# Kernel tuning notes

Hardware: AMD Instinct MI355X
Metric: run time of the kernel (lower is better)

The kernel has to match this reference:

```python
import jax, jax.numpy as jnp
import numpy as np

D_MODEL = 1024
N_STATE = 64
BASEWIDTH = 3
BC_SCALE = (D_MODEL / BASEWIDTH) ** -0.5  # 'mup' mode width_mult**-0.5
RMS_EPS = 1.1920928955078125e-07  # torch.finfo(float32).eps (RMSNorm eps=None default)


def setup_inputs() -> dict:
    key = jax.random.key(0)
    k1, k2, k3, k4 = jax.random.split(key, 4)
    Bsz, L = 4, 2048
    u = jax.random.normal(k1, (Bsz, D_MODEL, L), dtype=jnp.float32)
    A = jax.random.uniform(k2, (N_STATE,), dtype=jnp.float32) * 0.1  # buffer: rand(N)*A_scale
    B = (jax.random.normal(k3, (N_STATE, D_MODEL), dtype=jnp.float32) + 0.1) * BC_SCALE
    C = (jax.random.normal(k4, (N_STATE, D_MODEL), dtype=jnp.float32) + 0.1) * BC_SCALE
    D = jnp.ones((D_MODEL,), dtype=jnp.float32)
    norm_w = jnp.ones((D_MODEL,), dtype=jnp.float32)
    return {"L": L, "u": u, "A": A, "B": B, "C": C, "D": D, "norm_w": norm_w}


def _ssm(u, A, B, C, D, norm_w):
    # u: [b, d, l]
    scale = BC_SCALE  # applied to Bu, Cu in 'mup' hyperparam mode
    Bu = jnp.einsum('nd,bdl->bnl', B, u) * scale  # [b, n, l]
    Cu = jnp.einsum('nd,bdl->bnl', C, u) * scale  # [b, n, l]
    b, d, l = u.shape
    # shifted_delta == 1 (delta path commented out in source), so
    # h_{t} = A * h_{t-1} + Bu[:, :, t] (outer) u[:, :, t]
    h0 = jnp.zeros((b, d, A.shape[0]), dtype=u.dtype)

    def step(h, xs):
        bu_t, cu_t, u_t = xs  # [b,n], [b,n], [b,d]
        h = h * A + u_t[:, :, None] * bu_t[:, None, :]  # [b, d, n]
        y_t = jnp.einsum('bn,bdn->bd', cu_t, h)
        return h, y_t

    xs = (jnp.moveaxis(Bu, 2, 0), jnp.moveaxis(Cu, 2, 0), jnp.moveaxis(u, 2, 0))
    _, y = jax.lax.scan(step, h0, xs)  # y: [l, b, d]
    y = jnp.moveaxis(y, 0, 2).transpose(1, 0, 2) if False else jnp.transpose(y, (1, 2, 0))  # [b, d, l]
    out = y + u * D[None, :, None]
    # RMSNorm over d_model (apply in [b, l, d] layout)
    x = jnp.transpose(out, (0, 2, 1))  # [b, l, d]
    ms = jnp.mean(x * x, axis=-1, keepdims=True)
    x = x * jax.lax.rsqrt(ms + RMS_EPS) * norm_w
    return jnp.transpose(x, (0, 2, 1))  # [b, d, l]


def reference(L, u, A, B, C, D, norm_w):
    del L  # sequence length == u.shape[-1]
    return _ssm(u, A, B, C, D, norm_w)
```

## Files before the change

### kernel.cpp

```cpp
#include <hip/hip_runtime.h>
#include <stdint.h>

#define DM 1024
#define LS 2048
#define RMS_EPS 1.1920928955078125e-07f
#define S2 0.0029296875f

typedef __attribute__((ext_vector_type(8))) short bf16x8;
typedef __attribute__((ext_vector_type(4))) float f32x4;

__device__ __forceinline__ unsigned short f2bf(float f) {
  uint32_t u = __builtin_bit_cast(uint32_t, f);
  u += 0x7FFFu + ((u >> 16) & 1u);
  return (unsigned short)(u >> 16);
}

__global__ __launch_bounds__(256) void k0_prep(const float* __restrict__ B,
                                               const float* __restrict__ C,
                                               unsigned short* __restrict__ Bbf) {
  int i4 = blockIdx.x * 256 + threadIdx.x;
  const float4* src = (i4 < 16384) ? (const float4*)B : (const float4*)C;
  float4 v = src[i4 & 16383];
  ushort4 o;
  o.x = f2bf(v.x); o.y = f2bf(v.y); o.z = f2bf(v.z); o.w = f2bf(v.w);
  ((ushort4*)Bbf)[i4] = o;
}

__global__ __launch_bounds__(1024) void kf(const float* __restrict__ u,
                                           const unsigned short* __restrict__ Bbf,
                                           const float* __restrict__ A,
                                           const float* __restrict__ Dv,
                                           const float* __restrict__ nw,
                                           float* __restrict__ out) {
  const int wg  = blockIdx.x;
  const int nbx = (wg & 7) * 64 + (wg >> 3);
  const int b   = nbx >> 7;
  const int t0  = (nbx & 127) << 4;
  const int tid = threadIdx.x;
  const int lane = tid & 63;
  const int w    = tid >> 6;
  const float* ub = u + (size_t)b * DM * LS;
  float* ob = out + (size_t)b * DM * LS;

  __shared__ __align__(16) char SMEM[65536];
  __shared__ __align__(16) float Bu[32][68];
  __shared__ __align__(16) float Cu[16][68];
  __shared__ __align__(16) float KwS[16][20];
  bf16x8 (*tile)[32]  = (bf16x8 (*)[32])SMEM;
  float (*y_lds)[1024] = (float (*)[1024])SMEM;
  float (*SS2)[20] = (float (*)[20])Cu;
  float *rsq       = (float*)((char*)Cu + 1280);

  {
    const int h16 = w >> 3;
    const int ks  = w & 7;
    const int tb  = lane >> 5;
    const int kg  = (lane >> 2) & 7;
    const int lq  = lane & 3;
    const int kbase = 128*ks + 64*tb + 8*kg;
    const int gcol  = t0 - 16 + 16*h16 + 4*lq;
    float4 vv[8];
    if (gcol >= 0) {
      #pragma unroll
      for (int r = 0; r < 8; ++r)
        vv[r] = *(const float4*)(ub + (size_t)(kbase + r) * LS + gcol);
    } else {
      #pragma unroll
      for (int r = 0; r < 8; ++r) vv[r] = make_float4(0.f, 0.f, 0.f, 0.f);
    }
    const int k8 = 16*ks + 8*tb + kg;
    #pragma unroll
    for (int c = 0; c < 4; ++c) {
      union { bf16x8 v; unsigned short s[8]; } t8;
      #pragma unroll
      for (int r = 0; r < 8; ++r) t8.s[r] = f2bf(((const float*)&vv[r])[c]);
      tile[k8][16*h16 + ((4*lq + c) ^ (k8 & 3))] = t8.v;
    }
  }
  __syncthreads();

  {
    const int nn = lane & 15, q = lane >> 4;
    const int wm = w & 7, wn = w >> 3;
    const unsigned short* arow = Bbf + (size_t)(16*wm + nn) * DM;
    f32x4 acc = {};
    #pragma unroll 4
    for (int it = 0; it < 32; ++it) {
      bf16x8 bfrag = tile[4*it + q][16*wn + (nn ^ q)];
      bf16x8 afrag = *(const bf16x8*)(arow + 32*it + 8*q);
      acc = __builtin_amdgcn_mfma_f32_16x16x32_bf16(afrag, bfrag, acc, 0, 0, 0);
    }
    const int ucol = 16*wn + nn;
    const int bcr  = 16*wm + 4*q;
    if (wm < 4)       *(f32x4*)&Bu[ucol][bcr]            = acc;
    else if (wn == 1) *(f32x4*)&Cu[ucol - 16][bcr - 64]  = acc;
  }
  __syncthreads();

  {
    const int p  = lane & 15;
    const int tl = lane >> 4;
    const int jq = w & 3;
    const int t  = 4*(w >> 2) + tl;
    const float4 cu = *(const float4*)&Cu[t][4*p];
    const float4 aa = *(const float4*)(A + 4*p);
    float a2x = aa.x*aa.x, a2y = aa.y*aa.y, a2z = aa.z*aa.z, a2w = aa.w*aa.w;
    float a4x = a2x*a2x,  a4y = a2y*a2y,  a4z = a2z*a2z,  a4w = a2w*a2w;
    float a8x = a4x*a4x,  a8y = a4y*a4y,  a8z = a4z*a4z,  a8w = a4w*a4w;
    float acx = a8x*a4x,  acy = a8y*a4y,  acz = a8z*a4z,  acw = a8w*a4w;
    float apx = (jq==0)?1.f:(jq==1)?a4x:(jq==2)?a8x:acx;
    float apy = (jq==0)?1.f:(jq==1)?a4y:(jq==2)?a8y:acy;
    float apz = (jq==0)?1.f:(jq==1)?a4z:(jq==2)?a8z:acz;
    float apw = (jq==0)?1.f:(jq==1)?a4w:(jq==2)?a8w:acw;
    float pw0 = cu.x * S2 * apx;
    float pw1 = cu.y * S2 * apy;
    float pw2 = cu.z * S2 * apz;
    float pw3 = cu.w * S2 * apw;
    #pragma unroll
    for (int jj = 0; jj < 4; ++jj) {
      const int j = 4*jq + jj;
      const float4 b4 = *(const float4*)&Bu[16 + t - j][4*p];
      float s = pw0*b4.x + pw1*b4.y + pw2*b4.z + pw3*b4.w;
      s += __shfl_xor(s, 1, 64);
      s += __shfl_xor(s, 2, 64);
      s += __shfl_xor(s, 4, 64);
      s += __shfl_xor(s, 8, 64);
      if (p == 0) KwS[t][j] = s;
      pw0 *= aa.x; pw1 *= aa.y; pw2 *= aa.z; pw3 *= aa.w;
    }
  }
  __syncthreads();

  const int tg = tid & 3;
  const int dr = tid >> 2;
  const int cbase = t0 - 16 + 4*tg;
  float ps[4] = {0.f, 0.f, 0.f, 0.f};
  #pragma unroll 1
  for (int c = 0; c < 4; ++c) {
    const int d = dr + 256*c;
    const float* row = ub + (size_t)d * LS;
    float wr[20];
    #pragma unroll
    for (int s5 = 0; s5 < 5; ++s5) {
      int g = cbase + 4*s5;
      float4 v = (g >= 0) ? *(const float4*)(row + g)
                          : make_float4(0.f, 0.f, 0.f, 0.f);
      wr[4*s5+0] = v.x; wr[4*s5+1] = v.y; wr[4*s5+2] = v.z; wr[4*s5+3] = v.w;
    }
    const float Dd = Dv[d];
    #pragma unroll
    for (int k = 0; k < 4; ++k) {
      f32x4 kv0 = *(const f32x4*)&KwS[4*tg + k][0];
      f32x4 kv1 = *(const f32x4*)&KwS[4*tg + k][4];
      f32x4 kv2 = *(const f32x4*)&KwS[4*tg + k][8];
      f32x4 kv3 = *(const f32x4*)&KwS[4*tg + k][12];
      float acc = wr[16 + k] * Dd;
      #pragma unroll
      for (int j = 0; j < 4; ++j)  acc = fmaf(kv0[j], wr[16 + k - j],      acc);
      #pragma unroll
      for (int j = 0; j < 4; ++j)  acc = fmaf(kv1[j], wr[16 + k - (j+4)],  acc);
      #pragma unroll
      for (int j = 0; j < 4; ++j)  acc = fmaf(kv2[j], wr[16 + k - (j+8)],  acc);
      #pragma unroll
      for (int j = 0; j < 4; ++j)  acc = fmaf(kv3[j], wr[16 + k - (j+12)], acc);
      y_lds[4*tg + k][d] = acc;
      ps[k] = fmaf(acc, acc, ps[k]);
    }
  }
  #pragma unroll
  for (int k = 0; k < 4; ++k) {
    ps[k] += __shfl_xor(ps[k], 4, 64);
    ps[k] += __shfl_xor(ps[k], 8, 64);
    ps[k] += __shfl_xor(ps[k], 16, 64);
    ps[k] += __shfl_xor(ps[k], 32, 64);
  }
  if (lane < 4) {
    float4 o = make_float4(ps[0], ps[1], ps[2], ps[3]);
    *(float4*)&SS2[w][4*lane] = o;
  }
  __syncthreads();
  if (tid < 16) {
    float s = 0.f;
    #pragma unroll
    for (int ww = 0; ww < 16; ++ww) s += SS2[ww][tid];
    rsq[tid] = rsqrtf(s * (1.f/1024.f) + RMS_EPS);
  }
  __syncthreads();
  float rq[4];
  #pragma unroll
  for (int k = 0; k < 4; ++k) rq[k] = rsq[4*tg + k];
  #pragma unroll
  for (int c = 0; c < 4; ++c) {
    const int d = dr + 256*c;
    const float wn2 = nw[d];
    float4 o;
    o.x = y_lds[4*tg + 0][d] * rq[0] * wn2;
    o.y = y_lds[4*tg + 1][d] * rq[1] * wn2;
    o.z = y_lds[4*tg + 2][d] * rq[2] * wn2;
    o.w = y_lds[4*tg + 3][d] * rq[3] * wn2;
    *(float4*)(ob + (size_t)d * LS + t0 + 4*tg) = o;
  }
}

extern "C" void kernel_launch(void* const* d_in, const int* in_sizes, int n_in,
                              void* d_out, int out_size, void* d_ws, size_t ws_size,
                              hipStream_t stream) {
  const float* u  = (const float*)d_in[1];
  const float* A  = (const float*)d_in[2];
  const float* B  = (const float*)d_in[3];
  const float* C  = (const float*)d_in[4];
  const float* Dv = (const float*)d_in[5];
  const float* nw = (const float*)d_in[6];
  float* out = (float*)d_out;

  unsigned short* Bbf = (unsigned short*)d_ws;

  k0_prep<<<dim3(128), dim3(256),  0, stream>>>(B, C, Bbf);
  kf     <<<dim3(512), dim3(1024), 0, stream>>>(u, Bbf, A, Dv, nw, out);
}
```

Measured before the change: 145.1 us.

## Split fused kernel into separate Bu/Cu GEMM and convolution-norm kernels

The single fused kernel, which recomputed the Bu/Cu projection for each 16-step tile including a 16-step halo, is replaced by two kernels. The first computes Bu and Cu once for all time steps with a 64-column tiled, double-buffered MFMA GEMM and stores them transposed to workspace. The second reads that window, builds the 16-tap kernel weights, then applies the convolution and RMSNorm over 32 time steps in two halves. This removes the duplicated halo GEMM work and the B/C refetch per tile. In exchange it adds a global round trip for Bu/Cu and an extra launch, and each kernel runs fewer blocks.

```diff
diff --git a/kernel.cpp b/kernel.cpp
--- a/kernel.cpp
+++ b/kernel.cpp
@@ -26,100 +26,120 @@
   ((ushort4*)Bbf)[i4] = o;
 }
 
-__global__ __launch_bounds__(1024) void kf(const float* __restrict__ u,
-                                           const unsigned short* __restrict__ Bbf,
-                                           const float* __restrict__ A,
-                                           const float* __restrict__ Dv,
-                                           const float* __restrict__ nw,
-                                           float* __restrict__ out) {
-  const int wg  = blockIdx.x;
-  const int nbx = (wg & 7) * 64 + (wg >> 3);
-  const int b   = nbx >> 7;
-  const int t0  = (nbx & 127) << 4;
+__global__ __launch_bounds__(512) void kg(const float* __restrict__ u,
+                                          const unsigned short* __restrict__ Bbf,
+                                          float* __restrict__ BuCuT) {
+  const int b   = blockIdx.y;
+  const int l0  = blockIdx.x * 64;
+  const int tid = threadIdx.x;
+  const int lane = tid & 63;
+  const int w    = tid >> 6;
+  const float* ub = u + (size_t)b * DM * LS;
+
+  __shared__ bf16x8 At[128][8];
+  __shared__ float  Ut[64][68];
+
+  const int nn = lane & 15, q = lane >> 4;
+  const int wr = w >> 2, wc = w & 3;
+
+  bf16x8 arg[2]; float4 urg[2];
+
+  auto LOAD = [&](int kk) {
+    #pragma unroll
+    for (int j = 0; j < 2; ++j) {
+      int id = tid + 512*j;
+      arg[j] = *(const bf16x8*)(Bbf + (size_t)(id >> 3) * DM + 64*kk + 8*(id & 7));
+    }
+    #pragma unroll
+    for (int j = 0; j < 2; ++j) {
+      int id = tid + 512*j;
+      urg[j] = *(const float4*)(ub + (size_t)(64*kk + (id >> 4)) * LS + l0 + 4*(id & 15));
+    }
+  };
+  auto WRITE = [&]() {
+    #pragma unroll
+    for (int j = 0; j < 2; ++j) {
+      int id = tid + 512*j;
+      At[id >> 3][(id & 7) ^ ((id >> 3) & 7)] = arg[j];
+    }
+    #pragma unroll
+    for (int j = 0; j < 2; ++j) {
+      int id = tid + 512*j;
+      *(float4*)&Ut[id >> 4][4*(id & 15)] = urg[j];
+    }
+  };
+
+  f32x4 acc[4] = {};
+  LOAD(0); WRITE(); __syncthreads();
+
+  for (int kk = 0; kk < 16; ++kk) {
+    if (kk < 15) LOAD(kk + 1);
+    #pragma unroll
+    for (int c = 0; c < 2; ++c) {
+      union { bf16x8 v; unsigned short s[8]; } bf;
+      #pragma unroll
+      for (int jj = 0; jj < 8; ++jj)
+        bf.s[jj] = f2bf(Ut[32*c + 8*q + jj][16*wc + nn]);
+      #pragma unroll
+      for (int m = 0; m < 4; ++m) {
+        const int row = 64*wr + 16*m + nn;
+        bf16x8 af = At[row][(4*c + q) ^ (row & 7)];
+        acc[m] = __builtin_amdgcn_mfma_f32_16x16x32_bf16(af, bf.v, acc[m], 0, 0, 0);
+      }
+    }
+    __syncthreads();
+    if (kk < 15) { WRITE(); __syncthreads(); }
+  }
+
+  const int col = l0 + 16*wc + nn;
+  float* ob = BuCuT + ((size_t)b * LS + col) * 128;
+  #pragma unroll
+  for (int m = 0; m < 4; ++m)
+    *(f32x4*)(ob + 64*wr + 16*m + 4*q) = acc[m];
+}
+
+__global__ __launch_bounds__(512) void kc(const float* __restrict__ u,
+                                          const float* __restrict__ BuCuT,
+                                          const float* __restrict__ A,
+                                          const float* __restrict__ Dv,
+                                          const float* __restrict__ nw,
+                                          float* __restrict__ out) {
+  const int b   = blockIdx.y;
+  const int t0  = blockIdx.x * 32;
   const int tid = threadIdx.x;
   const int lane = tid & 63;
   const int w    = tid >> 6;
   const float* ub = u + (size_t)b * DM * LS;
   float* ob = out + (size_t)b * DM * LS;
 
-  __shared__ __align__(16) char SMEM[65536];
-  __shared__ __align__(16) float Bu[32][68];
-  __shared__ __align__(16) float Cu[16][68];
-  __shared__ __align__(16) float KwS[16][20];
-  bf16x8 (*tile)[32]  = (bf16x8 (*)[32])SMEM;
-  float (*y_lds)[1024] = (float (*)[1024])SMEM;
-  float (*SS2)[20] = (float (*)[20])Cu;
-  float *rsq       = (float*)((char*)Cu + 1280);
+  __shared__ __align__(16) char SMEM[66048];
+  float (*win)[132]  = (float (*)[132])SMEM;
+  float (*y_l)[1026] = (float (*)[1026])SMEM;
+  __shared__ float KwS[32][20];
+  __shared__ float SSr[8][16];
+  __shared__ float rsqv[16];
 
   {
-    const int h16 = w >> 3;
-    const int ks  = w & 7;
-    const int tb  = lane >> 5;
-    const int kg  = (lane >> 2) & 7;
-    const int lq  = lane & 3;
-    const int kbase = 128*ks + 64*tb + 8*kg;
-    const int gcol  = t0 - 16 + 16*h16 + 4*lq;
-    float4 vv[8];
-    if (gcol >= 0) {
-      #pragma unroll
-      for (int r = 0; r < 8; ++r)
-        vv[r] = *(const float4*)(ub + (size_t)(kbase + r) * LS + gcol);
-    } else {
-      #pragma unroll
-      for (int r = 0; r < 8; ++r) vv[r] = make_float4(0.f, 0.f, 0.f, 0.f);
-    }
-    const int k8 = 16*ks + 8*tb + kg;
-    #pragma unroll
-    for (int c = 0; c < 4; ++c) {
-      union { bf16x8 v; unsigned short s[8]; } t8;
-      #pragma unroll
-      for (int r = 0; r < 8; ++r) t8.s[r] = f2bf(((const float*)&vv[r])[c]);
-      tile[k8][16*h16 + ((4*lq + c) ^ (k8 & 3))] = t8.v;
+    #pragma unroll
+    for (int j = 0; j < 3; ++j) {
+      int id = tid + 512*j;
+      int r = id >> 5, c4 = id & 31;
+      int g = t0 - 16 + r;
+      float4 v = (g >= 0) ? *(const float4*)(BuCuT + ((size_t)b * LS + g) * 128 + 4*c4)
+                          : make_float4(0.f, 0.f, 0.f, 0.f);
+      *(float4*)&win[r][4*c4] = v;
     }
   }
   __syncthreads();
 
   {
-    const int nn = lane & 15, q = lane >> 4;
-    const int wm = w & 7, wn = w >> 3;
-    const unsigned short* arow = Bbf + (size_t)(16*wm + nn) * DM;
-    f32x4 acc = {};
-    #pragma unroll 4
-    for (int it = 0; it < 32; ++it) {
-      bf16x8 bfrag = tile[4*it + q][16*wn + (nn ^ q)];
-      bf16x8 afrag = *(const bf16x8*)(arow + 32*it + 8*q);
-      acc = __builtin_amdgcn_mfma_f32_16x16x32_bf16(afrag, bfrag, acc, 0, 0, 0);
-    }
-    const int ucol = 16*wn + nn;
-    const int bcr  = 16*wm + 4*q;
-    if (wm < 4)       *(f32x4*)&Bu[ucol][bcr]            = acc;
-    else if (wn == 1) *(f32x4*)&Cu[ucol - 16][bcr - 64]  = acc;
-  }
-  __syncthreads();
-
-  {
-    const int p  = lane & 15;
-    const int tl = lane >> 4;
-    const int jq = w & 3;
-    const int t  = 4*(w >> 2) + tl;
-    const float4 cu = *(const float4*)&Cu[t][4*p];
-    const float4 aa = *(const float4*)(A + 4*p);
-    float a2x = aa.x*aa.x, a2y = aa.y*aa.y, a2z = aa.z*aa.z, a2w = aa.w*aa.w;
-    float a4x = a2x*a2x,  a4y = a2y*a2y,  a4z = a2z*a2z,  a4w = a2w*a2w;
-    float a8x = a4x*a4x,  a8y = a4y*a4y,  a8z = a4z*a4z,  a8w = a4w*a4w;
-    float acx = a8x*a4x,  acy = a8y*a4y,  acz = a8z*a4z,  acw = a8w*a4w;
-    float apx = (jq==0)?1.f:(jq==1)?a4x:(jq==2)?a8x:acx;
-    float apy = (jq==0)?1.f:(jq==1)?a4y:(jq==2)?a8y:acy;
-    float apz = (jq==0)?1.f:(jq==1)?a4z:(jq==2)?a8z:acz;
-    float apw = (jq==0)?1.f:(jq==1)?a4w:(jq==2)?a8w:acw;
-    float pw0 = cu.x * S2 * apx;
-    float pw1 = cu.y * S2 * apy;
-    float pw2 = cu.z * S2 * apz;
-    float pw3 = cu.w * S2 * apw;
-    #pragma unroll
-    for (int jj = 0; jj < 4; ++jj) {
-      const int j = 4*jq + jj;
-      const float4 b4 = *(const float4*)&Bu[16 + t - j][4*p];
+    const int t = tid >> 4, p = tid & 15;
+    float4 cu = *(const float4*)&win[16 + t][64 + 4*p];
+    float4 aa = *(const float4*)(A + 4*p);
+    float pw0 = cu.x * S2, pw1 = cu.y * S2, pw2 = cu.z * S2, pw3 = cu.w * S2;
+    #pragma unroll
+    for (int j = 0; j < 16; ++j) {
+      float4 b4 = *(const float4*)&win[16 + t - j][4*p];
       float s = pw0*b4.x + pw1*b4.y + pw2*b4.z + pw3*b4.w;
       s += __shfl_xor(s, 1, 64);
       s += __shfl_xor(s, 2, 64);
@@ -131,74 +151,65 @@
   }
   __syncthreads();
 
-  const int tg = tid & 3;
+  const int cq = tid & 3;
   const int dr = tid >> 2;
-  const int cbase = t0 - 16 + 4*tg;
-  float ps[4] = {0.f, 0.f, 0.f, 0.f};
   #pragma unroll 1
-  for (int c = 0; c < 4; ++c) {
-    const int d = dr + 256*c;
-    const float* row = ub + (size_t)d * LS;
-    float wr[20];
-    #pragma unroll
-    for (int s5 = 0; s5 < 5; ++s5) {
-      int g = cbase + 4*s5;
-      float4 v = (g >= 0) ? *(const float4*)(row + g)
-                          : make_float4(0.f, 0.f, 0.f, 0.f);
-      wr[4*s5+0] = v.x; wr[4*s5+1] = v.y; wr[4*s5+2] = v.z; wr[4*s5+3] = v.w;
-    }
-    const float Dd = Dv[d];
+  for (int h = 0; h < 2; ++h) {
+    float ps[4] = {0.f, 0.f, 0.f, 0.f};
+    const int cbase = t0 + 16*h - 16 + 4*cq;
+    #pragma unroll 1
+    for (int c = 0; c < 8; ++c) {
+      const int d = dr + 128*c;
+      const float* row = ub + (size_t)d * LS;
+      float wrr[20];
+      #pragma unroll
+      for (int s5 = 0; s5 < 5; ++s5) {
+        int g = cbase + 4*s5;
+        float4 v = (g >= 0) ? *(const float4*)(row + g)
+                            : make_float4(0.f, 0.f, 0.f, 0.f);
+        wrr[4*s5+0] = v.x; wrr[4*s5+1] = v.y; wrr[4*s5+2] = v.z; wrr[4*s5+3] = v.w;
+      }
+      const float Dd = Dv[d];
+      #pragma unroll
+      for (int k = 0; k < 4; ++k) {
+        const float* kwp = &KwS[16*h + 4*cq + k][0];
+        float acc = wrr[16 + k] * Dd;
+        #pragma unroll
+        for (int j = 0; j < 16; ++j)
+          acc = fmaf(kwp[j], wrr[16 + k - j], acc);
+        y_l[4*cq + k][d] = acc;
+        ps[k] = fmaf(acc, acc, ps[k]);
+      }
+    }
     #pragma unroll
     for (int k = 0; k < 4; ++k) {
-      f32x4 kv0 = *(const f32x4*)&KwS[4*tg + k][0];
-      f32x4 kv1 = *(const f32x4*)&KwS[4*tg + k][4];
-      f32x4 kv2 = *(const f32x4*)&KwS[4*tg + k][8];
-      f32x4 kv3 = *(const f32x4*)&KwS[4*tg + k][12];
-      float acc = wr[16 + k] * Dd;
-      #pragma unroll
-      for (int j = 0; j < 4; ++j)  acc = fmaf(kv0[j], wr[16 + k - j],      acc);
-      #pragma unroll
-      for (int j = 0; j < 4; ++j)  acc = fmaf(kv1[j], wr[16 + k - (j+4)],  acc);
-      #pragma unroll
-      for (int j = 0; j < 4; ++j)  acc = fmaf(kv2[j], wr[16 + k - (j+8)],  acc);
-      #pragma unroll
-      for (int j = 0; j < 4; ++j)  acc = fmaf(kv3[j], wr[16 + k - (j+12)], acc);
-      y_lds[4*tg + k][d] = acc;
-      ps[k] = fmaf(acc, acc, ps[k]);
-    }
-  }
-  #pragma unroll
-  for (int k = 0; k < 4; ++k) {
-    ps[k] += __shfl_xor(ps[k], 4, 64);
-    ps[k] += __shfl_xor(ps[k], 8, 64);
-    ps[k] += __shfl_xor(ps[k], 16, 64);
-    ps[k] += __shfl_xor(ps[k], 32, 64);
-  }
-  if (lane < 4) {
-    float4 o = make_float4(ps[0], ps[1], ps[2], ps[3]);
-    *(float4*)&SS2[w][4*lane] = o;
-  }
-  __syncthreads();
-  if (tid < 16) {
-    float s = 0.f;
-    #pragma unroll
-    for (int ww = 0; ww < 16; ++ww) s += SS2[ww][tid];
-    rsq[tid] = rsqrtf(s * (1.f/1024.f) + RMS_EPS);
-  }
-  __syncthreads();
-  float rq[4];
-  #pragma unroll
-  for (int k = 0; k < 4; ++k) rq[k] = rsq[4*tg + k];
-  #pragma unroll
-  for (int c = 0; c < 4; ++c) {
-    const int d = dr + 256*c;
-    const float wn2 = nw[d];
-    float4 o;
-    o.x = y_lds[4*tg + 0][d] * rq[0] * wn2;
-    o.y = y_lds[4*tg + 1][d] * rq[1] * wn2;
-    o.z = y_lds[4*tg + 2][d] * rq[2] * wn2;
-    o.w = y_lds[4*tg + 3][d] * rq[3] * wn2;
-    *(float4*)(ob + (size_t)d * LS + t0 + 4*tg) = o;
+      ps[k] += __shfl_xor(ps[k], 4, 64);
+      ps[k] += __shfl_xor(ps[k], 8, 64);
+      ps[k] += __shfl_xor(ps[k], 16, 64);
+      ps[k] += __shfl_xor(ps[k], 32, 64);
+    }
+    if (lane < 4)
+      *(float4*)&SSr[w][4*lane] = make_float4(ps[0], ps[1], ps[2], ps[3]);
+    __syncthreads();
+    if (tid < 16) {
+      float s = 0.f;
+      #pragma unroll
+      for (int ww = 0; ww < 8; ++ww) s += SSr[ww][tid];
+      rsqv[tid] = rsqrtf(s * (1.f/1024.f) + RMS_EPS);
+    }
+    __syncthreads();
+    #pragma unroll 1
+    for (int c = 0; c < 8; ++c) {
+      const int d = dr + 128*c;
+      const float wn = nw[d];
+      float4 o;
+      o.x = y_l[4*cq + 0][d] * rsqv[4*cq + 0] * wn;
+      o.y = y_l[4*cq + 1][d] * rsqv[4*cq + 1] * wn;
+      o.z = y_l[4*cq + 2][d] * rsqv[4*cq + 2] * wn;
+      o.w = y_l[4*cq + 3][d] * rsqv[4*cq + 3] * wn;
+      *(float4*)(ob + (size_t)d * LS + t0 + 16*h + 4*cq) = o;
+    }
+    __syncthreads();
   }
 }
 
@@ -213,8 +224,10 @@
   const float* nw = (const float*)d_in[6];
   float* out = (float*)d_out;
 
-  unsigned short* Bbf = (unsigned short*)d_ws;
-
-  k0_prep<<<dim3(128), dim3(256),  0, stream>>>(B, C, Bbf);
-  kf     <<<dim3(512), dim3(1024), 0, stream>>>(u, Bbf, A, Dv, nw, out);
-}
+  float* BuCuT = (float*)d_ws;
+  unsigned short* Bbf = (unsigned short*)((char*)d_ws + (4u << 20));
+
+  k0_prep<<<dim3(128),    dim3(256), 0, stream>>>(B, C, Bbf);
+  kg     <<<dim3(32, 4),  dim3(512), 0, stream>>>(u, Bbf, BuCuT);
+  kc     <<<dim3(64, 4),  dim3(512), 0, stream>>>(u, BuCuT, A, Dv, nw, out);
+}
```

Result: slower. 161.3 us (+11.1%).

## Split fused SSM kernel into separate projection GEMM and convolution/norm kernels

Applied to the files above, without the earlier changes.

Replaces the single fused kernel, which recomputed Bu/Cu projections including a 16-step halo per tile, with a dedicated GEMM kernel that writes Bu and Cu to a global workspace in [b, l, 128] layout. A second kernel reads them to build the truncated decay kernel and does the causal convolution, skip term and RMSNorm. That kernel keeps per-thread outputs in registers instead of a 64KB LDS tile. The aim is to remove the redundant halo GEMM work and the large LDS footprint so occupancy improves, at the cost of an extra launch and a global round trip for Bu/Cu. u is also read twice from global memory.

```diff
diff --git a/kernel.cpp b/kernel.cpp
--- a/kernel.cpp
+++ b/kernel.cpp
@@ -26,100 +26,102 @@
   ((ushort4*)Bbf)[i4] = o;
 }
 
-__global__ __launch_bounds__(1024) void kf(const float* __restrict__ u,
-                                           const unsigned short* __restrict__ Bbf,
-                                           const float* __restrict__ A,
-                                           const float* __restrict__ Dv,
-                                           const float* __restrict__ nw,
-                                           float* __restrict__ out) {
-  const int wg  = blockIdx.x;
-  const int nbx = (wg & 7) * 64 + (wg >> 3);
-  const int b   = nbx >> 7;
-  const int t0  = (nbx & 127) << 4;
-  const int tid = threadIdx.x;
+__global__ __launch_bounds__(512) void kg(const float* __restrict__ u,
+                                          const unsigned short* __restrict__ Bbf,
+                                          float* __restrict__ BuCuT) {
+  const int wg = blockIdx.x;
+  const int sw = (wg & 7) * 64 + (wg >> 3);
+  const int mh = sw & 1;
+  const int lt = (sw >> 1) & 63;
+  const int b  = sw >> 7;
+  const int l0 = lt * 32;
+  const int tid  = threadIdx.x;
+  const int lane = tid & 63;
+  const int w    = tid >> 6;
+  const int nn = lane & 15, q = lane >> 4;
+  const int wm = w >> 1, wn = w & 1;
+
+  const float* ub = u + (size_t)b * DM * LS;
+  const int row  = 64*mh + 16*wm + nn;
+  const int ucol = l0 + 16*wn + nn;
+  const float* ubase = ub + ucol;
+  const unsigned short* abase = Bbf + (size_t)row * DM + 8*q;
+
+  f32x4 acc = {};
+  float uA[8], uB[8];
+  bf16x8 aA, aB;
+
+  auto LD = [&](int it, float* ur, bf16x8* ar) {
+    const float* p = ubase + (size_t)(32*it + 8*q) * LS;
+    #pragma unroll
+    for (int jj = 0; jj < 8; ++jj) ur[jj] = p[(size_t)jj * LS];
+    *ar = *(const bf16x8*)(abase + 32*it);
+  };
+  auto STEP = [&](const float* ur, const bf16x8* ar) {
+    union { bf16x8 v; unsigned short s[8]; } t8;
+    #pragma unroll
+    for (int jj = 0; jj < 8; ++jj) t8.s[jj] = f2bf(ur[jj]);
+    acc = __builtin_amdgcn_mfma_f32_16x16x32_bf16(*ar, t8.v, acc, 0, 0, 0);
+  };
+
+  LD(0, uA, &aA);
+  LD(1, uB, &aB);
+  #pragma unroll
+  for (int it = 0; it < 16; ++it) {
+    STEP(uA, &aA);
+    if (it < 15) LD(2*it + 2, uA, &aA);
+    STEP(uB, &aB);
+    if (it < 15) LD(2*it + 3, uB, &aB);
+  }
+
+  const int col = l0 + 16*wn + nn;
+  float* ob = BuCuT + ((size_t)b * LS + col) * 128;
+  *(f32x4*)(ob + 64*mh + 16*wm + 4*q) = acc;
+}
+
+__global__ __launch_bounds__(512) void kc(const float* __restrict__ u,
+                                          const float* __restrict__ BuCuT,
+                                          const float* __restrict__ A,
+                                          const float* __restrict__ Dv,
+                                          const float* __restrict__ nw,
+                                          float* __restrict__ out) {
+  const int wg = blockIdx.x;
+  const int sw = (wg & 7) * 64 + (wg >> 3);
+  const int b  = sw >> 7;
+  const int t0 = (sw & 127) * 16;
+  const int tid  = threadIdx.x;
   const int lane = tid & 63;
   const int w    = tid >> 6;
   const float* ub = u + (size_t)b * DM * LS;
   float* ob = out + (size_t)b * DM * LS;
 
-  __shared__ __align__(16) char SMEM[65536];
-  __shared__ __align__(16) float Bu[32][68];
-  __shared__ __align__(16) float Cu[16][68];
-  __shared__ __align__(16) float KwS[16][20];
-  bf16x8 (*tile)[32]  = (bf16x8 (*)[32])SMEM;
-  float (*y_lds)[1024] = (float (*)[1024])SMEM;
-  float (*SS2)[20] = (float (*)[20])Cu;
-  float *rsq       = (float*)((char*)Cu + 1280);
+  __shared__ float KwS[16][20];
+  __shared__ float SSr[8][16];
+  __shared__ float rsqv[16];
 
   {
-    const int h16 = w >> 3;
-    const int ks  = w & 7;
-    const int tb  = lane >> 5;
-    const int kg  = (lane >> 2) & 7;
-    const int lq  = lane & 3;
-    const int kbase = 128*ks + 64*tb + 8*kg;
-    const int gcol  = t0 - 16 + 16*h16 + 4*lq;
-    float4 vv[8];
-    if (gcol >= 0) {
-      #pragma unroll
-      for (int r = 0; r < 8; ++r)
-        vv[r] = *(const float4*)(ub + (size_t)(kbase + r) * LS + gcol);
-    } else {
-      #pragma unroll
-      for (int r = 0; r < 8; ++r) vv[r] = make_float4(0.f, 0.f, 0.f, 0.f);
-    }
-    const int k8 = 16*ks + 8*tb + kg;
-    #pragma unroll
-    for (int c = 0; c < 4; ++c) {
-      union { bf16x8 v; unsigned short s[8]; } t8;
-      #pragma unroll
-      for (int r = 0; r < 8; ++r) t8.s[r] = f2bf(((const float*)&vv[r])[c]);
-      tile[k8][16*h16 + ((4*lq + c) ^ (k8 & 3))] = t8.v;
-    }
-  }
-  __syncthreads();
-
-  {
-    const int nn = lane & 15, q = lane >> 4;
-    const int wm = w & 7, wn = w >> 3;
-    const unsigned short* arow = Bbf + (size_t)(16*wm + nn) * DM;
-    f32x4 acc = {};
-    #pragma unroll 4
-    for (int it = 0; it < 32; ++it) {
-      bf16x8 bfrag = tile[4*it + q][16*wn + (nn ^ q)];
-      bf16x8 afrag = *(const bf16x8*)(arow + 32*it + 8*q);
-      acc = __builtin_amdgcn_mfma_f32_16x16x32_bf16(afrag, bfrag, acc, 0, 0, 0);
-    }
-    const int ucol = 16*wn + nn;
-    const int bcr  = 16*wm + 4*q;
-    if (wm < 4)       *(f32x4*)&Bu[ucol][bcr]            = acc;
-    else if (wn == 1) *(f32x4*)&Cu[ucol - 16][bcr - 64]  = acc;
-  }
-  __syncthreads();
-
-  {
-    const int p  = lane & 15;
-    const int tl = lane >> 4;
-    const int jq = w & 3;
-    const int t  = 4*(w >> 2) + tl;
-    const float4 cu = *(const float4*)&Cu[t][4*p];
+    const int t  = (tid >> 4) & 15;
+    const int p  = tid & 15;
+    const int jh = tid >> 8;
+    const float* bb = BuCuT + (size_t)b * LS * 128;
+    const float4 cu = *(const float4*)(bb + (size_t)(t0 + t) * 128 + 64 + 4*p);
     const float4 aa = *(const float4*)(A + 4*p);
-    float a2x = aa.x*aa.x, a2y = aa.y*aa.y, a2z = aa.z*aa.z, a2w = aa.w*aa.w;
-    float a4x = a2x*a2x,  a4y = a2y*a2y,  a4z = a2z*a2z,  a4w = a2w*a2w;
-    float a8x = a4x*a4x,  a8y = a4y*a4y,  a8z = a4z*a4z,  a8w = a4w*a4w;
-    float acx = a8x*a4x,  acy = a8y*a4y,  acz = a8z*a4z,  acw = a8w*a4w;
-    float apx = (jq==0)?1.f:(jq==1)?a4x:(jq==2)?a8x:acx;
-    float apy = (jq==0)?1.f:(jq==1)?a4y:(jq==2)?a8y:acy;
-    float apz = (jq==0)?1.f:(jq==1)?a4z:(jq==2)?a8z:acz;
-    float apw = (jq==0)?1.f:(jq==1)?a4w:(jq==2)?a8w:acw;
+    float apx = 1.f, apy = 1.f, apz = 1.f, apw = 1.f;
+    if (jh) {
+      float a2x = aa.x*aa.x, a2y = aa.y*aa.y, a2z = aa.z*aa.z, a2w = aa.w*aa.w;
+      float a4x = a2x*a2x,  a4y = a2y*a2y,  a4z = a2z*a2z,  a4w = a2w*a2w;
+      apx = a4x*a4x; apy = a4y*a4y; apz = a4z*a4z; apw = a4w*a4w;
+    }
     float pw0 = cu.x * S2 * apx;
     float pw1 = cu.y * S2 * apy;
     float pw2 = cu.z * S2 * apz;
     float pw3 = cu.w * S2 * apw;
     #pragma unroll
-    for (int jj = 0; jj < 4; ++jj) {
-      const int j = 4*jq + jj;
-      const float4 b4 = *(const float4*)&Bu[16 + t - j][4*p];
+    for (int jj = 0; jj < 8; ++jj) {
+      const int j = 8*jh + jj;
+      const int g = t0 + t - j;
+      float4 b4 = (g >= 0) ? *(const float4*)(bb + (size_t)g * 128 + 4*p)
+                           : make_float4(0.f, 0.f, 0.f, 0.f);
       float s = pw0*b4.x + pw1*b4.y + pw2*b4.z + pw3*b4.w;
       s += __shfl_xor(s, 1, 64);
       s += __shfl_xor(s, 2, 64);
@@ -134,16 +136,17 @@
   const int tg = tid & 3;
   const int dr = tid >> 2;
   const int cbase = t0 - 16 + 4*tg;
+  float y[8][4];
   float ps[4] = {0.f, 0.f, 0.f, 0.f};
   #pragma unroll 1
-  for (int c = 0; c < 4; ++c) {
-    const int d = dr + 256*c;
-    const float* row = ub + (size_t)d * LS;
+  for (int c = 0; c < 8; ++c) {
+    const int d = dr + 128*c;
+    const float* rowp = ub + (size_t)d * LS;
     float wr[20];
     #pragma unroll
     for (int s5 = 0; s5 < 5; ++s5) {
       int g = cbase + 4*s5;
-      float4 v = (g >= 0) ? *(const float4*)(row + g)
+      float4 v = (g >= 0) ? *(const float4*)(rowp + g)
                           : make_float4(0.f, 0.f, 0.f, 0.f);
       wr[4*s5+0] = v.x; wr[4*s5+1] = v.y; wr[4*s5+2] = v.z; wr[4*s5+3] = v.w;
     }
@@ -163,10 +166,11 @@
       for (int j = 0; j < 4; ++j)  acc = fmaf(kv2[j], wr[16 + k - (j+8)],  acc);
       #pragma unroll
       for (int j = 0; j < 4; ++j)  acc = fmaf(kv3[j], wr[16 + k - (j+12)], acc);
-      y_lds[4*tg + k][d] = acc;
+      y[c][k] = acc;
       ps[k] = fmaf(acc, acc, ps[k]);
     }
   }
+
   #pragma unroll
   for (int k = 0; k < 4; ++k) {
     ps[k] += __shfl_xor(ps[k], 4, 64);
@@ -174,30 +178,29 @@
     ps[k] += __shfl_xor(ps[k], 16, 64);
     ps[k] += __shfl_xor(ps[k], 32, 64);
   }
-  if (lane < 4) {
-    float4 o = make_float4(ps[0], ps[1], ps[2], ps[3]);
-    *(float4*)&SS2[w][4*lane] = o;
-  }
+  if (lane < 4)
+    *(float4*)&SSr[w][4*lane] = make_float4(ps[0], ps[1], ps[2], ps[3]);
   __syncthreads();
   if (tid < 16) {
     float s = 0.f;
     #pragma unroll
-    for (int ww = 0; ww < 16; ++ww) s += SS2[ww][tid];
-    rsq[tid] = rsqrtf(s * (1.f/1024.f) + RMS_EPS);
+    for (int ww = 0; ww < 8; ++ww) s += SSr[ww][tid];
+    rsqv[tid] = rsqrtf(s * (1.f/1024.f) + RMS_EPS);
   }
   __syncthreads();
+
   float rq[4];
   #pragma unroll
-  for (int k = 0; k < 4; ++k) rq[k] = rsq[4*tg + k];
-  #pragma unroll
-  for (int c = 0; c < 4; ++c) {
-    const int d = dr + 256*c;
+  for (int k = 0; k < 4; ++k) rq[k] = rsqv[4*tg + k];
+  #pragma unroll 1
+  for (int c = 0; c < 8; ++c) {
+    const int d = dr + 128*c;
     const float wn2 = nw[d];
     float4 o;
-    o.x = y_lds[4*tg + 0][d] * rq[0] * wn2;
-    o.y = y_lds[4*tg + 1][d] * rq[1] * wn2;
-    o.z = y_lds[4*tg + 2][d] * rq[2] * wn2;
-    o.w = y_lds[4*tg + 3][d] * rq[3] * wn2;
+    o.x = y[c][0] * rq[0] * wn2;
+    o.y = y[c][1] * rq[1] * wn2;
+    o.z = y[c][2] * rq[2] * wn2;
+    o.w = y[c][3] * rq[3] * wn2;
     *(float4*)(ob + (size_t)d * LS + t0 + 4*tg) = o;
   }
 }
@@ -213,8 +216,10 @@
   const float* nw = (const float*)d_in[6];
   float* out = (float*)d_out;
 
-  unsigned short* Bbf = (unsigned short*)d_ws;
-
-  k0_prep<<<dim3(128), dim3(256),  0, stream>>>(B, C, Bbf);
-  kf     <<<dim3(512), dim3(1024), 0, stream>>>(u, Bbf, A, Dv, nw, out);
-}
+  float* BuCuT = (float*)d_ws;
+  unsigned short* Bbf = (unsigned short*)((char*)d_ws + (4u << 20));
+
+  k0_prep<<<dim3(128), dim3(256), 0, stream>>>(B, C, Bbf);
+  kg     <<<dim3(512), dim3(512), 0, stream>>>(u, Bbf, BuCuT);
+  kc     <<<dim3(512), dim3(512), 0, stream>>>(u, BuCuT, A, Dv, nw, out);
+}
```

Measured after the change: 152.9 us. 1.05x slower.
